# Kernel tuning notes

Measured on AMD Instinct MI355X. Metric: run time of the kernel, lower is better.

Reference implementation:

```python
import jax, jax.numpy as jnp
import numpy as np

PH = PW = PD = 8  # patch dims from patch_config


def setup_inputs() -> dict:
    key = jax.random.key(0)
    image = jax.random.normal(key, (2, 1, 256, 256, 64), dtype=jnp.float32)
    return {"image": image, "n": 8}


def _extract_patches(image):
    # image: [B, C, H, W, D] -> features [B, N, C*PH*PW*PD]
    # matches torch loop order: height blocks outer, then width, then depth;
    # per-patch flatten order is (C, h, w, d) via reshape(B, 1, -1)
    B, C, H, W, D = image.shape
    Hb, Wb, Db = H // PH, W // PW, D // PD
    x = image.reshape(B, C, Hb, PH, Wb, PW, Db, PD)
    x = x.transpose(0, 2, 4, 6, 1, 3, 5, 7)  # [B, Hb, Wb, Db, C, PH, PW, PD]
    return x.reshape(B, Hb * Wb * Db, C * PH * PW * PD)


def reference(image, n):
    feats = _extract_patches(image)          # [B, N, F]
    B, N, F = feats.shape
    # pairwise squared euclidean distances (monotone in distance -> same kNN)
    sq = jnp.sum(feats * feats, axis=-1)      # [B, N]
    d2 = sq[:, :, None] + sq[:, None, :] - 2.0 * jnp.einsum('bnf,bmf->bnm', feats, feats)
    # sklearn kneighbors_graph excludes self (include_self=False)
    d2 = jnp.where(jnp.eye(N, dtype=bool)[None], jnp.inf, d2)
    _, idx = jax.lax.top_k(-d2, n)            # [B, N, n] nearest neighbor indices
    b = jnp.arange(B)[:, None, None]
    r = jnp.arange(N)[None, :, None]
    adj = jnp.zeros((B, N, N), dtype=feats.dtype).at[b, r, idx].set(1.0)
    adj = (adj + adj.transpose(0, 2, 1)) * 0.5  # symmetrize as (A + A^T)/2
    return feats, adj
```

## Files before the change

kernel.cpp:

```cpp
#include <hip/hip_runtime.h>
#include <float.h>

#define NPTS  8192
#define FDIM  512
#define NB    2
#define TK    12
#define KNN   8
#define NQ    4

typedef __attribute__((ext_vector_type(8))) short short8;
typedef __attribute__((ext_vector_type(4))) float floatx4;

__device__ __forceinline__ unsigned f2bf(float x) {
    unsigned u = __float_as_uint(x);
    return (u + 0x7FFFu + ((u >> 16) & 1u)) >> 16;
}

__global__ void extract_prep_kernel(const float* __restrict__ img, float* __restrict__ feats,
                                    ushort* __restrict__ bf, float* __restrict__ sqc16) {
    __shared__ float part[4];
    const int tid = threadIdx.x;
    int t = blockIdx.x * 256 + tid;
    int fq = t & 127;
    int p  = (t >> 7) & 8191;
    int b  = t >> 20;
    int f = fq << 2;
    int d = f & 7;
    int w = (f >> 3) & 7;
    int h = f >> 6;
    int db = p & 7, wb = (p >> 3) & 31, hb = p >> 8;
    size_t src = (((size_t)(b * 256 + hb * 8 + h)) * 256 + (size_t)(wb * 8 + w)) * 64
               + (size_t)(db * 8 + d);
    float4 v = *(const float4*)(img + src);
    *(float4*)(feats + ((size_t)t << 2)) = v;
    uint2 wv;
    wv.x = f2bf(v.x) | (f2bf(v.y) << 16);
    wv.y = f2bf(v.z) | (f2bf(v.w) << 16);
    *(uint2*)(bf + ((size_t)t << 2)) = wv;
    float s = v.x * v.x + v.y * v.y + v.z * v.z + v.w * v.w;
#pragma unroll
    for (int off = 32; off > 0; off >>= 1) s += __shfl_xor(s, off);
    if ((tid & 63) == 0) part[tid >> 6] = s;
    __syncthreads();
    if (tid < 2) {
        int gw = blockIdx.x * 2 + tid;
        sqc16[gw] = (part[2 * tid] + part[2 * tid + 1]) * 16.f + 24576.f;
    }
}

__device__ __forceinline__ void insert12(unsigned* L, unsigned key) {
#pragma unroll
    for (int p = TK - 1; p > 0; --p) {
        bool bp = key < L[p - 1];
        bool bc = key < L[p];
        L[p] = bp ? L[p - 1] : (bc ? key : L[p]);
    }
    L[0] = (key < L[0]) ? key : L[0];
}

__device__ __forceinline__ int swz(int x) { return (x & 3) ^ ((x >> 2) & 3); }

__device__ __forceinline__ unsigned pkminu16(unsigned a, unsigned b) {
    unsigned d;
    asm("v_pk_min_u16 %0, %1, %2" : "=v"(d) : "v"(a), "v"(b));
    return d;
}

__device__ __forceinline__ void gl_lds16(const ushort* g, ushort* l) {
    __builtin_amdgcn_global_load_lds(
        (const __attribute__((address_space(1))) unsigned int*)g,
        (__attribute__((address_space(3))) unsigned int*)l, 16, 0, 0);
}

__global__ __launch_bounds__(256, 2)
void knn_mfma(const ushort* __restrict__ bfeats, const float* __restrict__ sqc16,
              unsigned* __restrict__ cand) {
    __shared__ __align__(16) ushort As[128 * 32];
    __shared__ __align__(16) ushort Bs[256 * 32];
    __shared__ __align__(16) ushort Sc[64 * 264];

    const int row0 = blockIdx.x * 128;
    const int b    = blockIdx.y;
    const int quarter = blockIdx.z;
    const ushort* bfb = bfeats + (size_t)b * NPTS * FDIM;
    const float*  sqg = sqc16 + b * NPTS;

    const int tid  = threadIdx.x;
    const int wid  = tid >> 6;
    const int lane = tid & 63;
    const int l15  = lane & 15;
    const int q    = lane >> 4;
    const int wr   = wid & 1;
    const int wc   = wid >> 1;

    const int fsw = (q ^ swz(l15)) << 3;
    int aoff[4], boff[8];
#pragma unroll
    for (int rf = 0; rf < 4; ++rf) aoff[rf] = ((wr * 64 + rf * 16 + l15) << 5) + fsw;
#pragma unroll
    for (int cf = 0; cf < 8; ++cf) boff[cf] = ((wc * 128 + cf * 16 + l15) << 5) + fsw;

    const int srl = lane >> 2;
    const int sg  = (lane & 3) ^ swz(srl);

    unsigned L[2][TK];
#pragma unroll
    for (int h = 0; h < 2; ++h)
#pragma unroll
        for (int s = 0; s < TK; ++s) L[h][s] = 0xFFFFFFFFu;

    const int srow = tid >> 2;
    const int scp  = tid & 3;

    for (int ct = 0; ct < 8; ++ct) {
        const int colb = quarter * 2048 + ct * 256;

        float sqv[8];
#pragma unroll
        for (int cf = 0; cf < 8; ++cf) sqv[cf] = sqg[colb + wc * 128 + cf * 16 + l15];

        floatx4 acc[4][8];
#pragma unroll
        for (int rf = 0; rf < 4; ++rf)
#pragma unroll
            for (int cf = 0; cf < 8; ++cf) acc[rf][cf] = (floatx4)0.f;

        for (int kt = 0; kt < 16; ++kt) {
            const int kb = kt * 32;
            __syncthreads();
#pragma unroll
            for (int p = 0; p < 2; ++p) {
                int rg = wid * 2 + p;
                gl_lds16(bfb + (size_t)(row0 + rg * 16 + srl) * FDIM + kb + sg * 8,
                         &As[rg * 512]);
            }
#pragma unroll
            for (int p = 0; p < 4; ++p) {
                int cg = wid * 4 + p;
                gl_lds16(bfb + (size_t)(colb + cg * 16 + srl) * FDIM + kb + sg * 8,
                         &Bs[cg * 512]);
            }
            __syncthreads();

            short8 av[4], bv[8];
#pragma unroll
            for (int rf = 0; rf < 4; ++rf) av[rf] = *(const short8*)&As[aoff[rf]];
#pragma unroll
            for (int cf = 0; cf < 8; ++cf) bv[cf] = *(const short8*)&Bs[boff[cf]];
#pragma unroll
            for (int rf = 0; rf < 4; ++rf)
#pragma unroll
                for (int cf = 0; cf < 8; ++cf)
                    acc[rf][cf] = __builtin_amdgcn_mfma_f32_16x16x32_bf16(
                        av[rf], bv[cf], acc[rf][cf], 0, 0, 0);
        }

#pragma unroll
        for (int hr = 0; hr < 2; ++hr) {
            __syncthreads();
            if (wr == hr) {
#pragma unroll
                for (int rf = 0; rf < 4; ++rf)
#pragma unroll
                    for (int cf = 0; cf < 8; ++cf) {
                        const int ctl = wc * 128 + cf * 16 + l15;
                        const int gcol = colb + ctl;
#pragma unroll
                        for (int v = 0; v < 4; ++v) {
                            const int rbuf = rf * 16 + q * 4 + v;
                            const int grow = row0 + hr * 64 + rbuf;
                            float s = fmaf(-32.f, acc[rf][cf][v], sqv[cf]);
                            s = fminf(fmaxf(s, 0.f), 65535.f);
                            ushort us = (grow == gcol) ? (ushort)65535 : (ushort)s;
                            Sc[rbuf * 264 + ctl] = us;
                        }
                    }
            }
            __syncthreads();
            const ushort* base = &Sc[srow * 264 + scp * 64];
            const int colg0 = colb + scp * 64;
            unsigned* Lp = L[hr];
#pragma unroll
            for (int j = 0; j < 8; ++j) {
                uint4 w = *(const uint4*)(base + j * 8);
                unsigned m = pkminu16(pkminu16(w.x, w.y), pkminu16(w.z, w.w));
                unsigned mm = min(m & 0xFFFFu, m >> 16);
                unsigned thr = Lp[TK - 1] >> 16;
                if (mm <= thr) {
                    const int c0 = colg0 + j * 8;
                    unsigned k;
                    k = (w.x << 16) | (unsigned)(c0 + 0); if (k < Lp[TK-1]) insert12(Lp, k);
                    k = (w.x & 0xFFFF0000u) | (unsigned)(c0 + 1); if (k < Lp[TK-1]) insert12(Lp, k);
                    k = (w.y << 16) | (unsigned)(c0 + 2); if (k < Lp[TK-1]) insert12(Lp, k);
                    k = (w.y & 0xFFFF0000u) | (unsigned)(c0 + 3); if (k < Lp[TK-1]) insert12(Lp, k);
                    k = (w.z << 16) | (unsigned)(c0 + 4); if (k < Lp[TK-1]) insert12(Lp, k);
                    k = (w.z & 0xFFFF0000u) | (unsigned)(c0 + 5); if (k < Lp[TK-1]) insert12(Lp, k);
                    k = (w.w << 16) | (unsigned)(c0 + 6); if (k < Lp[TK-1]) insert12(Lp, k);
                    k = (w.w & 0xFFFF0000u) | (unsigned)(c0 + 7); if (k < Lp[TK-1]) insert12(Lp, k);
                }
            }
        }
    }

#pragma unroll
    for (int m = 1; m <= 2; m <<= 1) {
#pragma unroll
        for (int h = 0; h < 2; ++h) {
            unsigned o[TK];
#pragma unroll
            for (int s = 0; s < TK; ++s) o[s] = (unsigned)__shfl_xor((int)L[h][s], m);
#pragma unroll
            for (int s = 0; s < TK; ++s)
                if (o[s] < L[h][TK - 1]) insert12(L[h], o[s]);
        }
    }

    if (scp == 0) {
#pragma unroll
        for (int h = 0; h < 2; ++h) {
            const int grow = row0 + h * 64 + srow;
            unsigned* dst = cand + ((size_t)(b * NQ + quarter) * NPTS + grow) * TK;
#pragma unroll
            for (int s = 0; s < TK; ++s) dst[s] = L[h][s];
        }
    }
}

__global__ void refine_kernel(const float* __restrict__ feats, const unsigned* __restrict__ cand,
                              float* __restrict__ adj) {
    __shared__ unsigned scols[4][TK];
    const int wv   = threadIdx.x >> 6;
    const int lane = threadIdx.x & 63;
    const int gw = blockIdx.x * 4 + wv;
    const int b = gw >> 13;
    const int r = gw & (NPTS - 1);

    unsigned key = 0xFFFFFFFFu;
    if (lane < NQ * TK) {
        int qf = lane / TK, s = lane % TK;
        key = cand[((size_t)(b * NQ + qf) * NPTS + r) * TK + s];
    }
    int rank = 0;
#pragma unroll
    for (int u = 0; u < NQ * TK; ++u) {
        unsigned ku = (unsigned)__shfl((int)key, u);
        rank += (ku < key) ? 1 : 0;
    }
    if (lane < NQ * TK && rank < TK) scols[wv][rank] = key & 0xFFFFu;
    __syncthreads();

    const float* fb = feats + (size_t)b * NPTS * FDIM;
    const float* fr = fb + (size_t)r * FDIM + lane * 8;
    float* adjb = adj + (size_t)b * NPTS * NPTS;

    float4 a0 = *(const float4*)fr;
    float4 a1 = *(const float4*)(fr + 4);

    double dist[TK];
#pragma unroll
    for (int t = 0; t < TK; ++t) {
        int c = (int)scols[wv][t];
        const float* fc = fb + (size_t)c * FDIM + lane * 8;
        float4 c0 = *(const float4*)fc;
        float4 c1 = *(const float4*)(fc + 4);
        double sm = 0.0, e;
        e = (double)a0.x - (double)c0.x; sm += e * e;
        e = (double)a0.y - (double)c0.y; sm += e * e;
        e = (double)a0.z - (double)c0.z; sm += e * e;
        e = (double)a0.w - (double)c0.w; sm += e * e;
        e = (double)a1.x - (double)c1.x; sm += e * e;
        e = (double)a1.y - (double)c1.y; sm += e * e;
        e = (double)a1.z - (double)c1.z; sm += e * e;
        e = (double)a1.w - (double)c1.w; sm += e * e;
#pragma unroll
        for (int off = 32; off > 0; off >>= 1) sm += __shfl_xor(sm, off);
        dist[t] = sm;
    }

    if (lane < TK) {
        const int t = lane;
        const int ct = (int)scols[wv][t];
        int rk = 0;
#pragma unroll
        for (int u = 0; u < TK; ++u) {
            int cu = (int)scols[wv][u];
            rk += (dist[u] < dist[t]) || (dist[u] == dist[t] && cu < ct);
        }
        if (rk < KNN) {
            atomicAdd(&adjb[(size_t)r * NPTS + ct], 0.5f);
            atomicAdd(&adjb[(size_t)ct * NPTS + r], 0.5f);
        }
    }
}

extern "C" void kernel_launch(void* const* d_in, const int* in_sizes, int n_in,
                              void* d_out, int out_size, void* d_ws, size_t ws_size,
                              hipStream_t stream) {
    (void)in_sizes; (void)n_in; (void)out_size; (void)ws_size;
    const float* img = (const float*)d_in[0];

    float* feats = (float*)d_out;
    float* adj   = feats + (size_t)NB * NPTS * FDIM;

    float*    sqc16 = (float*)d_ws;
    unsigned* cand  = (unsigned*)((char*)d_ws + 65536);
    ushort*   bfeat = (ushort*)adj;

    extract_prep_kernel<<<8192, 256, 0, stream>>>(img, feats, bfeat, sqc16);
    knn_mfma      <<<dim3(NPTS / 128, NB, NQ), 256, 0, stream>>>(bfeat, sqc16, cand);
    (void)hipMemsetAsync(adj, 0, (size_t)NB * NPTS * NPTS * sizeof(float), stream);
    refine_kernel <<<(NB * NPTS) / 4, 256, 0, stream>>>(feats, cand, adj);
}
```

Baseline: 954.6 us.

## Double K-tile depth to 64, split selection into quarter-row passes, batch refine loads

New measurement: 1.082 ms. 13.3% more time.

```diff
diff --git a/kernel.cpp b/kernel.cpp
--- a/kernel.cpp
+++ b/kernel.cpp
@@ -58,8 +58,6 @@
     L[0] = (key < L[0]) ? key : L[0];
 }
 
-__device__ __forceinline__ int swz(int x) { return (x & 3) ^ ((x >> 2) & 3); }
-
 __device__ __forceinline__ unsigned pkminu16(unsigned a, unsigned b) {
     unsigned d;
     asm("v_pk_min_u16 %0, %1, %2" : "=v"(d) : "v"(a), "v"(b));
@@ -75,9 +73,9 @@
 __global__ __launch_bounds__(256, 2)
 void knn_mfma(const ushort* __restrict__ bfeats, const float* __restrict__ sqc16,
               unsigned* __restrict__ cand) {
-    __shared__ __align__(16) ushort As[128 * 32];
-    __shared__ __align__(16) ushort Bs[256 * 32];
-    __shared__ __align__(16) ushort Sc[64 * 264];
+    __shared__ __align__(16) ushort As[128 * 64];
+    __shared__ __align__(16) ushort Bs[256 * 64];
+    __shared__ __align__(16) ushort Sc[32 * 264];
 
     const int row0 = blockIdx.x * 128;
     const int b    = blockIdx.y;
@@ -92,25 +90,25 @@
     const int q    = lane >> 4;
     const int wr   = wid & 1;
     const int wc   = wid >> 1;
-
-    const int fsw = (q ^ swz(l15)) << 3;
-    int aoff[4], boff[8];
-#pragma unroll
-    for (int rf = 0; rf < 4; ++rf) aoff[rf] = ((wr * 64 + rf * 16 + l15) << 5) + fsw;
-#pragma unroll
-    for (int cf = 0; cf < 8; ++cf) boff[cf] = ((wc * 128 + cf * 16 + l15) << 5) + fsw;
-
-    const int srl = lane >> 2;
-    const int sg  = (lane & 3) ^ swz(srl);
-
-    unsigned L[2][TK];
-#pragma unroll
-    for (int h = 0; h < 2; ++h)
+    const int h8   = l15 & 7;
+
+    const int srl8 = lane >> 3;
+    const int sg8  = (lane & 7) ^ srl8;
+
+    int rowA[4], rowB[8];
+#pragma unroll
+    for (int rf = 0; rf < 4; ++rf) rowA[rf] = (wr * 64 + rf * 16 + l15) << 6;
+#pragma unroll
+    for (int cf = 0; cf < 8; ++cf) rowB[cf] = (wc * 128 + cf * 16 + l15) << 6;
+
+    unsigned L[4][TK];
+#pragma unroll
+    for (int h = 0; h < 4; ++h)
 #pragma unroll
         for (int s = 0; s < TK; ++s) L[h][s] = 0xFFFFFFFFu;
 
-    const int srow = tid >> 2;
-    const int scp  = tid & 3;
+    const int srow = tid >> 3;
+    const int scp  = tid & 7;
 
     for (int ct = 0; ct < 8; ++ct) {
         const int colb = quarter * 2048 + ct * 256;
@@ -125,63 +123,69 @@
 #pragma unroll
             for (int cf = 0; cf < 8; ++cf) acc[rf][cf] = (floatx4)0.f;
 
-        for (int kt = 0; kt < 16; ++kt) {
-            const int kb = kt * 32;
+        for (int kt = 0; kt < 8; ++kt) {
+            const int kb = kt * 64;
             __syncthreads();
 #pragma unroll
-            for (int p = 0; p < 2; ++p) {
-                int rg = wid * 2 + p;
-                gl_lds16(bfb + (size_t)(row0 + rg * 16 + srl) * FDIM + kb + sg * 8,
+            for (int p = 0; p < 4; ++p) {
+                int rg = wid * 4 + p;
+                gl_lds16(bfb + (size_t)(row0 + rg * 8 + srl8) * FDIM + kb + sg8 * 8,
                          &As[rg * 512]);
             }
 #pragma unroll
-            for (int p = 0; p < 4; ++p) {
-                int cg = wid * 4 + p;
-                gl_lds16(bfb + (size_t)(colb + cg * 16 + srl) * FDIM + kb + sg * 8,
+            for (int p = 0; p < 8; ++p) {
+                int cg = wid * 8 + p;
+                gl_lds16(bfb + (size_t)(colb + cg * 8 + srl8) * FDIM + kb + sg8 * 8,
                          &Bs[cg * 512]);
             }
             __syncthreads();
 
-            short8 av[4], bv[8];
-#pragma unroll
-            for (int rf = 0; rf < 4; ++rf) av[rf] = *(const short8*)&As[aoff[rf]];
-#pragma unroll
-            for (int cf = 0; cf < 8; ++cf) bv[cf] = *(const short8*)&Bs[boff[cf]];
-#pragma unroll
-            for (int rf = 0; rf < 4; ++rf)
-#pragma unroll
-                for (int cf = 0; cf < 8; ++cf)
-                    acc[rf][cf] = __builtin_amdgcn_mfma_f32_16x16x32_bf16(
-                        av[rf], bv[cf], acc[rf][cf], 0, 0, 0);
-        }
-
-#pragma unroll
-        for (int hr = 0; hr < 2; ++hr) {
+#pragma unroll
+            for (int ks = 0; ks < 2; ++ks) {
+                const int gsw = (((ks << 2) + q) ^ h8) << 3;
+                short8 av[4], bv[8];
+#pragma unroll
+                for (int rf = 0; rf < 4; ++rf) av[rf] = *(const short8*)&As[rowA[rf] + gsw];
+#pragma unroll
+                for (int cf = 0; cf < 8; ++cf) bv[cf] = *(const short8*)&Bs[rowB[cf] + gsw];
+#pragma unroll
+                for (int rf = 0; rf < 4; ++rf)
+#pragma unroll
+                    for (int cf = 0; cf < 8; ++cf)
+                        acc[rf][cf] = __builtin_amdgcn_mfma_f32_16x16x32_bf16(
+                            av[rf], bv[cf], acc[rf][cf], 0, 0, 0);
+            }
+        }
+
+#pragma unroll
+        for (int hr = 0; hr < 4; ++hr) {
             __syncthreads();
-            if (wr == hr) {
-#pragma unroll
-                for (int rf = 0; rf < 4; ++rf)
+            if (wr == (hr >> 1)) {
+#pragma unroll
+                for (int rr = 0; rr < 2; ++rr) {
+                    const int rf = (hr & 1) * 2 + rr;
 #pragma unroll
                     for (int cf = 0; cf < 8; ++cf) {
                         const int ctl = wc * 128 + cf * 16 + l15;
                         const int gcol = colb + ctl;
 #pragma unroll
                         for (int v = 0; v < 4; ++v) {
-                            const int rbuf = rf * 16 + q * 4 + v;
-                            const int grow = row0 + hr * 64 + rbuf;
+                            const int rbuf = rr * 16 + q * 4 + v;
+                            const int grow = row0 + hr * 32 + rbuf;
                             float s = fmaf(-32.f, acc[rf][cf][v], sqv[cf]);
                             s = fminf(fmaxf(s, 0.f), 65535.f);
                             ushort us = (grow == gcol) ? (ushort)65535 : (ushort)s;
                             Sc[rbuf * 264 + ctl] = us;
                         }
                     }
+                }
             }
             __syncthreads();
-            const ushort* base = &Sc[srow * 264 + scp * 64];
-            const int colg0 = colb + scp * 64;
+            const ushort* base = &Sc[srow * 264 + scp * 32];
+            const int colg0 = colb + scp * 32;
             unsigned* Lp = L[hr];
 #pragma unroll
-            for (int j = 0; j < 8; ++j) {
+            for (int j = 0; j < 4; ++j) {
                 uint4 w = *(const uint4*)(base + j * 8);
                 unsigned m = pkminu16(pkminu16(w.x, w.y), pkminu16(w.z, w.w));
                 unsigned mm = min(m & 0xFFFFu, m >> 16);
@@ -203,9 +207,9 @@
     }
 
 #pragma unroll
-    for (int m = 1; m <= 2; m <<= 1) {
-#pragma unroll
-        for (int h = 0; h < 2; ++h) {
+    for (int m = 1; m <= 4; m <<= 1) {
+#pragma unroll
+        for (int h = 0; h < 4; ++h) {
             unsigned o[TK];
 #pragma unroll
             for (int s = 0; s < TK; ++s) o[s] = (unsigned)__shfl_xor((int)L[h][s], m);
@@ -217,8 +221,8 @@
 
     if (scp == 0) {
 #pragma unroll
-        for (int h = 0; h < 2; ++h) {
-            const int grow = row0 + h * 64 + srow;
+        for (int h = 0; h < 4; ++h) {
+            const int grow = row0 + h * 32 + srow;
             unsigned* dst = cand + ((size_t)(b * NQ + quarter) * NPTS + grow) * TK;
 #pragma unroll
             for (int s = 0; s < TK; ++s) dst[s] = L[h][s];
@@ -258,23 +262,30 @@
 
     double dist[TK];
 #pragma unroll
-    for (int t = 0; t < TK; ++t) {
-        int c = (int)scols[wv][t];
-        const float* fc = fb + (size_t)c * FDIM + lane * 8;
-        float4 c0 = *(const float4*)fc;
-        float4 c1 = *(const float4*)(fc + 4);
-        double sm = 0.0, e;
-        e = (double)a0.x - (double)c0.x; sm += e * e;
-        e = (double)a0.y - (double)c0.y; sm += e * e;
-        e = (double)a0.z - (double)c0.z; sm += e * e;
-        e = (double)a0.w - (double)c0.w; sm += e * e;
-        e = (double)a1.x - (double)c1.x; sm += e * e;
-        e = (double)a1.y - (double)c1.y; sm += e * e;
-        e = (double)a1.z - (double)c1.z; sm += e * e;
-        e = (double)a1.w - (double)c1.w; sm += e * e;
-#pragma unroll
-        for (int off = 32; off > 0; off >>= 1) sm += __shfl_xor(sm, off);
-        dist[t] = sm;
+    for (int g = 0; g < TK / 4; ++g) {
+        float4 c0[4], c1[4];
+#pragma unroll
+        for (int i = 0; i < 4; ++i) {
+            int c = (int)scols[wv][g * 4 + i];
+            const float* fc = fb + (size_t)c * FDIM + lane * 8;
+            c0[i] = *(const float4*)fc;
+            c1[i] = *(const float4*)(fc + 4);
+        }
+#pragma unroll
+        for (int i = 0; i < 4; ++i) {
+            double sm = 0.0, e;
+            e = (double)a0.x - (double)c0[i].x; sm += e * e;
+            e = (double)a0.y - (double)c0[i].y; sm += e * e;
+            e = (double)a0.z - (double)c0[i].z; sm += e * e;
+            e = (double)a0.w - (double)c0[i].w; sm += e * e;
+            e = (double)a1.x - (double)c1[i].x; sm += e * e;
+            e = (double)a1.y - (double)c1[i].y; sm += e * e;
+            e = (double)a1.z - (double)c1[i].z; sm += e * e;
+            e = (double)a1.w - (double)c1[i].w; sm += e * e;
+#pragma unroll
+            for (int off = 32; off > 0; off >>= 1) sm += __shfl_xor(sm, off);
+            dist[g * 4 + i] = sm;
+        }
     }
 
     if (lane < TK) {
```

## Fuse adjacency zeroing into kNN MFMA kernel and batch refine feature loads

Applied to the files above, without the earlier changes.

Result: faster. 884.3 us (-7.4%).

```diff
diff --git a/kernel.cpp b/kernel.cpp
--- a/kernel.cpp
+++ b/kernel.cpp
@@ -74,7 +74,7 @@
 
 __global__ __launch_bounds__(256, 2)
 void knn_mfma(const ushort* __restrict__ bfeats, const float* __restrict__ sqc16,
-              unsigned* __restrict__ cand) {
+              unsigned* __restrict__ cand, float* __restrict__ adj) {
     __shared__ __align__(16) ushort As[128 * 32];
     __shared__ __align__(16) ushort Bs[256 * 32];
     __shared__ __align__(16) ushort Sc[64 * 264];
@@ -93,6 +93,10 @@
     const int wr   = wid & 1;
     const int wc   = wid >> 1;
 
+    const int blin = blockIdx.x + 64 * (blockIdx.y + NB * blockIdx.z);
+    float4* zbase = (float4*)adj + (size_t)blin * 65536;
+    const float4 zero4 = {0.f, 0.f, 0.f, 0.f};
+
     const int fsw = (q ^ swz(l15)) << 3;
     int aoff[4], boff[8];
 #pragma unroll
@@ -139,6 +143,11 @@
                 int cg = wid * 4 + p;
                 gl_lds16(bfb + (size_t)(colb + cg * 16 + srl) * FDIM + kb + sg * 8,
                          &Bs[cg * 512]);
+            }
+            {
+                const int it = ct * 16 + kt;
+                zbase[it * 512 + tid]       = zero4;
+                zbase[it * 512 + 256 + tid] = zero4;
             }
             __syncthreads();
 
@@ -258,23 +267,30 @@
 
     double dist[TK];
 #pragma unroll
-    for (int t = 0; t < TK; ++t) {
-        int c = (int)scols[wv][t];
-        const float* fc = fb + (size_t)c * FDIM + lane * 8;
-        float4 c0 = *(const float4*)fc;
-        float4 c1 = *(const float4*)(fc + 4);
-        double sm = 0.0, e;
-        e = (double)a0.x - (double)c0.x; sm += e * e;
-        e = (double)a0.y - (double)c0.y; sm += e * e;
-        e = (double)a0.z - (double)c0.z; sm += e * e;
-        e = (double)a0.w - (double)c0.w; sm += e * e;
-        e = (double)a1.x - (double)c1.x; sm += e * e;
-        e = (double)a1.y - (double)c1.y; sm += e * e;
-        e = (double)a1.z - (double)c1.z; sm += e * e;
-        e = (double)a1.w - (double)c1.w; sm += e * e;
-#pragma unroll
-        for (int off = 32; off > 0; off >>= 1) sm += __shfl_xor(sm, off);
-        dist[t] = sm;
+    for (int g = 0; g < TK / 4; ++g) {
+        float4 c0[4], c1[4];
+#pragma unroll
+        for (int i = 0; i < 4; ++i) {
+            int c = (int)scols[wv][g * 4 + i];
+            const float* fc = fb + (size_t)c * FDIM + lane * 8;
+            c0[i] = *(const float4*)fc;
+            c1[i] = *(const float4*)(fc + 4);
+        }
+#pragma unroll
+        for (int i = 0; i < 4; ++i) {
+            double sm = 0.0, e;
+            e = (double)a0.x - (double)c0[i].x; sm += e * e;
+            e = (double)a0.y - (double)c0[i].y; sm += e * e;
+            e = (double)a0.z - (double)c0[i].z; sm += e * e;
+            e = (double)a0.w - (double)c0[i].w; sm += e * e;
+            e = (double)a1.x - (double)c1[i].x; sm += e * e;
+            e = (double)a1.y - (double)c1[i].y; sm += e * e;
+            e = (double)a1.z - (double)c1[i].z; sm += e * e;
+            e = (double)a1.w - (double)c1[i].w; sm += e * e;
+#pragma unroll
+            for (int off = 32; off > 0; off >>= 1) sm += __shfl_xor(sm, off);
+            dist[g * 4 + i] = sm;
+        }
     }
 
     if (lane < TK) {
@@ -304,10 +320,9 @@
 
     float*    sqc16 = (float*)d_ws;
     unsigned* cand  = (unsigned*)((char*)d_ws + 65536);
-    ushort*   bfeat = (ushort*)adj;
+    ushort*   bfeat = (ushort*)((char*)d_ws + (16u << 20));
 
     extract_prep_kernel<<<8192, 256, 0, stream>>>(img, feats, bfeat, sqc16);
-    knn_mfma      <<<dim3(NPTS / 128, NB, NQ), 256, 0, stream>>>(bfeat, sqc16, cand);
-    (void)hipMemsetAsync(adj, 0, (size_t)NB * NPTS * NPTS * sizeof(float), stream);
+    knn_mfma      <<<dim3(NPTS / 128, NB, NQ), 256, 0, stream>>>(bfeat, sqc16, cand, adj);
     refine_kernel <<<(NB * NPTS) / 4, 256, 0, stream>>>(feats, cand, adj);
 }
```
